# Optimization experiments

Hardware: AMD Instinct MI355X
Metric: run time of the kernel (lower is better)

The kernel has to match this reference:

```python
import jax, jax.numpy as jnp
import numpy as np

DIM = 1024
HEADS = 16
HEAD_DIM = DIM // HEADS
MAX_SEQ = 4096
BATCH = 16
POSITION = MAX_SEQ - 1


def setup_inputs() -> dict:
    key = jax.random.key(0)
    ks = jax.random.split(key, 8)
    s = 0.02  # weight init scale, typical for transformer linears
    return {
        "token": jax.random.normal(ks[0], (BATCH, 1, DIM), dtype=jnp.float32),
        "k_cache": jax.random.normal(ks[1], (BATCH, MAX_SEQ, HEADS, HEAD_DIM), dtype=jnp.float32),
        "v_cache": jax.random.normal(ks[2], (BATCH, MAX_SEQ, HEADS, HEAD_DIM), dtype=jnp.float32),
        "Wq": jax.random.normal(ks[3], (DIM, DIM), dtype=jnp.float32) * s,
        "Wk": jax.random.normal(ks[4], (DIM, DIM), dtype=jnp.float32) * s,
        "Wv": jax.random.normal(ks[5], (DIM, DIM), dtype=jnp.float32) * s,
        "Wo": jax.random.normal(ks[6], (DIM, DIM), dtype=jnp.float32) * s,
        "position": POSITION,
    }


def reference(token, k_cache, v_cache, Wq, Wk, Wv, Wo, position):
    # Decode step: single-query attention against KV cache (FlexDecodingModule.decode).
    B = token.shape[0]
    # QKV projections (torch Linear: x @ W.T), bias=False
    q = (token @ Wq.T).reshape(B, 1, HEADS, HEAD_DIM)
    k = (token @ Wk.T).reshape(B, 1, HEADS, HEAD_DIM)
    v = (token @ Wv.T).reshape(B, 1, HEADS, HEAD_DIM)
    # Inline KV-cache append at `position` (static python int)
    kc = k_cache.at[:, position].set(k[:, 0])
    vc = v_cache.at[:, position].set(v[:, 0])
    past_k = kc[:, : position + 1]  # [B, L, H, D]
    past_v = vc[:, : position + 1]
    # Causal score_mod with offset=position, q_idx=0 => all kv_idx<=position visible (no mask)
    scale = 1.0 / np.sqrt(HEAD_DIM).astype(np.float32)
    scores = jnp.einsum("bqhd,bkhd->bhqk", q, past_k) * scale  # [B, H, 1, L]
    attn = jax.nn.softmax(scores, axis=-1)
    out = jnp.einsum("bhqk,bkhd->bqhd", attn, past_v)  # [B, 1, H, D]
    out = out.reshape(B, 1, DIM)
    return out @ Wo.T
```

## Files before the change

kernel.cpp:

```cpp
#include <hip/hip_runtime.h>
#include <hip/hip_bf16.h>
#include <math.h>

#define DIM 1024
#define HEADS 16
#define HEAD_DIM 64
#define MAXSEQ 4096
#define BATCH 16
#define CHUNK 1024
#define NCHUNK (MAXSEQ / CHUNK)

__global__ __launch_bounds__(256) void qkv_proj(
    const float* __restrict__ token,
    const float* __restrict__ Wq, const float* __restrict__ Wk,
    const float* __restrict__ Wv,
    float* __restrict__ out ) {
  __shared__ float tok[BATCH * DIM];
  for (int idx = threadIdx.x; idx < BATCH * DIM; idx += 256)
    tok[idx] = token[idx];
  __syncthreads();

  const float* W = (blockIdx.y == 0) ? Wq : ((blockIdx.y == 1) ? Wk : Wv);
  float* o = out + (size_t)blockIdx.y * BATCH * DIM;

  const int wave = threadIdx.x >> 6;
  const int lane = threadIdx.x & 63;
  const int i0 = blockIdx.x * 16 + wave * 4;

  float acc[4][16];
#pragma unroll
  for (int ii = 0; ii < 4; ++ii)
#pragma unroll
    for (int b = 0; b < 16; ++b) acc[ii][b] = 0.f;

  for (int t = 0; t < 16; ++t) {
    const int j = t * 64 + lane;
    float tk[16];
#pragma unroll
    for (int b = 0; b < 16; ++b) tk[b] = tok[b * DIM + j];
#pragma unroll
    for (int ii = 0; ii < 4; ++ii) {
      const float w = W[(size_t)(i0 + ii) * DIM + j];
#pragma unroll
      for (int b = 0; b < 16; ++b) acc[ii][b] = fmaf(w, tk[b], acc[ii][b]);
    }
  }

#pragma unroll
  for (int ii = 0; ii < 4; ++ii)
#pragma unroll
    for (int b = 0; b < 16; ++b) {
      float v = acc[ii][b];
#pragma unroll
      for (int m = 32; m >= 1; m >>= 1) v += __shfl_xor(v, m);
      if (lane == 0) o[(size_t)b * DIM + i0 + ii] = v;
    }
}

__global__ __launch_bounds__(256) void attn_partial(
    const float* __restrict__ kc, const float* __restrict__ vc,
    const float* __restrict__ qkv, const int* __restrict__ pos_p,
    float* __restrict__ part) {
  const int c = blockIdx.x, h = blockIdx.y, b = blockIdx.z;
  const int tid = threadIdx.x;
  const int wave = tid >> 6, lane = tid & 63;
  const int quarter = lane >> 4, lq = lane & 15;
  const int pos = pos_p[0];
  const int nk = pos + 1;
  const int s0 = c * CHUNK;

  const float* q = qkv + (size_t)b * DIM + h * HEAD_DIM;
  const float* knew = qkv + 1 * BATCH * DIM + (size_t)b * DIM + h * HEAD_DIM;
  const float* vnew = qkv + 2 * BATCH * DIM + (size_t)b * DIM + h * HEAD_DIM;
  const float* kbase = kc + (size_t)b * MAXSEQ * DIM + h * HEAD_DIM;
  const float* vbase = vc + (size_t)b * MAXSEQ * DIM + h * HEAD_DIM;

  const float scale = 0.125f;
  float4 q4 = *(const float4*)(q + lq * 4);
  q4.x *= scale; q4.y *= scale; q4.z *= scale; q4.w *= scale;

  __shared__ float sc[CHUNK];
  __shared__ float wred[4];
  __shared__ __align__(16) float vout[4][64];

#pragma unroll 4
  for (int it = 0; it < 64; ++it) {
    const int sl = wave * 256 + it * 4 + quarter;
    const int s = s0 + sl;
    const bool valid = (s < nk);
    float d = 0.f;
    if (valid) {
      const float* krow = (s == pos) ? knew : (kbase + (size_t)s * DIM);
      const float4 k4 = *(const float4*)(krow + lq * 4);
      d = q4.x * k4.x + q4.y * k4.y + q4.z * k4.z + q4.w * k4.w;
    }
    d += __shfl_xor(d, 1);
    d += __shfl_xor(d, 2);
    d += __shfl_xor(d, 4);
    d += __shfl_xor(d, 8);
    if (lq == 0) sc[sl] = valid ? d : -INFINITY;
  }
  __syncthreads();

  float lm = -INFINITY;
#pragma unroll
  for (int r = 0; r < 4; ++r) lm = fmaxf(lm, sc[tid + r * 256]);
#pragma unroll
  for (int m = 32; m >= 1; m >>= 1) lm = fmaxf(lm, __shfl_xor(lm, m));
  if (lane == 0) wred[wave] = lm;
  __syncthreads();
  const float m = fmaxf(fmaxf(wred[0], wred[1]), fmaxf(wred[2], wred[3]));
  __syncthreads();

  float lsum = 0.f;
#pragma unroll
  for (int r = 0; r < 4; ++r) {
    const int idx = tid + r * 256;
    const float s = sc[idx];
    const float p = (s == -INFINITY) ? 0.f : __expf(s - m);
    lsum += p;
    sc[idx] = p;
  }
#pragma unroll
  for (int mm = 32; mm >= 1; mm >>= 1) lsum += __shfl_xor(lsum, mm);
  __syncthreads();
  if (lane == 0) wred[wave] = lsum;
  __syncthreads();
  const float ltot = wred[0] + wred[1] + wred[2] + wred[3];

  float4 a4 = make_float4(0.f, 0.f, 0.f, 0.f);
#pragma unroll 4
  for (int it = 0; it < 64; ++it) {
    const int sl = wave * 256 + it * 4 + quarter;
    const int s = s0 + sl;
    if (s < nk) {
      const float* vrow = (s == pos) ? vnew : (vbase + (size_t)s * DIM);
      const float4 v4 = *(const float4*)(vrow + lq * 4);
      const float p = sc[sl];
      a4.x = fmaf(p, v4.x, a4.x);
      a4.y = fmaf(p, v4.y, a4.y);
      a4.z = fmaf(p, v4.z, a4.z);
      a4.w = fmaf(p, v4.w, a4.w);
    }
  }
  a4.x += __shfl_xor(a4.x, 16); a4.x += __shfl_xor(a4.x, 32);
  a4.y += __shfl_xor(a4.y, 16); a4.y += __shfl_xor(a4.y, 32);
  a4.z += __shfl_xor(a4.z, 16); a4.z += __shfl_xor(a4.z, 32);
  a4.w += __shfl_xor(a4.w, 16); a4.w += __shfl_xor(a4.w, 32);
  if (quarter == 0) *(float4*)(&vout[wave][lq * 4]) = a4;
  __syncthreads();

  const size_t base = (((size_t)(b * HEADS + h)) * NCHUNK + c) * 66;
  if (tid < 64) {
    const float a = vout[0][tid] + vout[1][tid] + vout[2][tid] + vout[3][tid];
    part[base + 2 + tid] = a;
  }
  if (tid == 0) { part[base] = m; part[base + 1] = ltot; }
}

__global__ __launch_bounds__(64) void attn_combine(
    const float* __restrict__ part, float* __restrict__ attn) {
  const int bh = blockIdx.x;
  const int b = bh >> 4, h = bh & 15;
  const int d = threadIdx.x;
  const float* p0 = part + (size_t)bh * NCHUNK * 66;
  float M = -INFINITY;
#pragma unroll
  for (int c = 0; c < NCHUNK; ++c) M = fmaxf(M, p0[c * 66]);
  float L = 0.f, o = 0.f;
#pragma unroll
  for (int c = 0; c < NCHUNK; ++c) {
    const float mc = p0[c * 66];
    if (mc > -INFINITY) {
      const float w = __expf(mc - M);
      L += p0[c * 66 + 1] * w;
      o = fmaf(p0[c * 66 + 2 + d], w, o);
    }
  }
  attn[(size_t)b * DIM + h * HEAD_DIM + d] = o / L;
}

__global__ __launch_bounds__(256) void o_proj(
    const float* __restrict__ attn, const float* __restrict__ Wo,
    float* __restrict__ out) {
  __shared__ float tok[BATCH * DIM];
  for (int idx = threadIdx.x; idx < BATCH * DIM; idx += 256)
    tok[idx] = attn[idx];
  __syncthreads();

  const int wave = threadIdx.x >> 6;
  const int lane = threadIdx.x & 63;
  const int i0 = blockIdx.x * 16 + wave * 4;

  float acc[4][16];
#pragma unroll
  for (int ii = 0; ii < 4; ++ii)
#pragma unroll
    for (int b = 0; b < 16; ++b) acc[ii][b] = 0.f;

  for (int t = 0; t < 16; ++t) {
    const int j = t * 64 + lane;
    float tk[16];
#pragma unroll
    for (int b = 0; b < 16; ++b) tk[b] = tok[b * DIM + j];
#pragma unroll
    for (int ii = 0; ii < 4; ++ii) {
      const float w = Wo[(size_t)(i0 + ii) * DIM + j];
#pragma unroll
      for (int b = 0; b < 16; ++b) acc[ii][b] = fmaf(w, tk[b], acc[ii][b]);
    }
  }

#pragma unroll
  for (int ii = 0; ii < 4; ++ii)
#pragma unroll
    for (int b = 0; b < 16; ++b) {
      float v = acc[ii][b];
#pragma unroll
      for (int m = 32; m >= 1; m >>= 1) v += __shfl_xor(v, m);
      if (lane == 0) out[(size_t)b * DIM + i0 + ii] = v;
    }
}

extern "C" void kernel_launch(void* const* d_in, const int* in_sizes, int n_in,
                              void* d_out, int out_size, void* d_ws, size_t ws_size,
                              hipStream_t stream) {
  const float* token = (const float*)d_in[0];
  const float* kc = (const float*)d_in[1];
  const float* vc = (const float*)d_in[2];
  const float* Wq = (const float*)d_in[3];
  const float* Wk = (const float*)d_in[4];
  const float* Wv = (const float*)d_in[5];
  const float* Wv_ = (const float*)d_in[5];
  const float* Wo = (const float*)d_in[6];
  const int* pos = (const int*)d_in[7];
  float* out = (float*)d_out;
  float* ws = (float*)d_ws;

  float* qkv = ws;
  float* part = ws + 3 * BATCH * DIM;
  float* attn = part + (size_t)BATCH * HEADS * NCHUNK * 66;

  hipLaunchKernelGGL(qkv_proj, dim3(64, 3), dim3(256), 0, stream,
                     token, Wq, Wk, Wv, qkv);
  hipLaunchKernelGGL(attn_partial, dim3(NCHUNK, HEADS, BATCH), dim3(256), 0,
                     stream, kc, vc, qkv, pos, part);
  hipLaunchKernelGGL(attn_combine, dim3(BATCH * HEADS), dim3(64), 0, stream,
                     part, attn);
  hipLaunchKernelGGL(o_proj, dim3(64), dim3(256), 0, stream, attn, Wo, out);
  (void)Wv_; (void)in_sizes; (void)n_in; (void)out_size; (void)ws_size;
}
```

Before: 160.1 us.

## Restructure attention partials so each block covers all heads over short contiguous chunks

The split-KV attention kernel now gives each block one batch element and a 64-row chunk across all 16 heads, instead of one head over a 1024-row chunk. Each thread handles one float4 of a full 4KB cache row, so every row load is one contiguous 4KB read rather than a 256B slice strided by the row pitch. Softmax reductions now run per head within 16-lane groups using a padded shared score tile, which drops the cross-wave reductions and several barriers. The cost is 16 times more partial results (per chunk, per head) for the combine kernel to merge, plus a larger workspace, and fewer rows in flight per thread.

```diff
diff --git a/kernel.cpp b/kernel.cpp
--- a/kernel.cpp
+++ b/kernel.cpp
@@ -7,7 +7,7 @@
 #define HEAD_DIM 64
 #define MAXSEQ 4096
 #define BATCH 16
-#define CHUNK 1024
+#define CHUNK 64
 #define NCHUNK (MAXSEQ / CHUNK)
 
 __global__ __launch_bounds__(256) void qkv_proj(
@@ -61,101 +61,88 @@
     const float* __restrict__ kc, const float* __restrict__ vc,
     const float* __restrict__ qkv, const int* __restrict__ pos_p,
     float* __restrict__ part) {
-  const int c = blockIdx.x, h = blockIdx.y, b = blockIdx.z;
-  const int tid = threadIdx.x;
-  const int wave = tid >> 6, lane = tid & 63;
-  const int quarter = lane >> 4, lq = lane & 15;
+  const int c = blockIdx.x, b = blockIdx.y;
+  const int t = threadIdx.x;
+  const int h = t >> 4, lq = t & 15;
   const int pos = pos_p[0];
   const int nk = pos + 1;
   const int s0 = c * CHUNK;
 
-  const float* q = qkv + (size_t)b * DIM + h * HEAD_DIM;
-  const float* knew = qkv + 1 * BATCH * DIM + (size_t)b * DIM + h * HEAD_DIM;
-  const float* vnew = qkv + 2 * BATCH * DIM + (size_t)b * DIM + h * HEAD_DIM;
-  const float* kbase = kc + (size_t)b * MAXSEQ * DIM + h * HEAD_DIM;
-  const float* vbase = vc + (size_t)b * MAXSEQ * DIM + h * HEAD_DIM;
+  const float* qp   = qkv + (size_t)b * DIM;
+  const float* knew = qkv + (size_t)BATCH * DIM + (size_t)b * DIM;
+  const float* vnew = qkv + 2 * (size_t)BATCH * DIM + (size_t)b * DIM;
+  const float* kbase = kc + (size_t)b * MAXSEQ * DIM;
+  const float* vbase = vc + (size_t)b * MAXSEQ * DIM;
 
   const float scale = 0.125f;
-  float4 q4 = *(const float4*)(q + lq * 4);
+  float4 q4 = *(const float4*)(qp + 4 * t);
   q4.x *= scale; q4.y *= scale; q4.z *= scale; q4.w *= scale;
 
-  __shared__ float sc[CHUNK];
-  __shared__ float wred[4];
-  __shared__ __align__(16) float vout[4][64];
+  __shared__ float sc[CHUNK][17];
 
 #pragma unroll 4
-  for (int it = 0; it < 64; ++it) {
-    const int sl = wave * 256 + it * 4 + quarter;
-    const int s = s0 + sl;
+  for (int i = 0; i < CHUNK; ++i) {
+    const int s = s0 + i;
     const bool valid = (s < nk);
     float d = 0.f;
     if (valid) {
       const float* krow = (s == pos) ? knew : (kbase + (size_t)s * DIM);
-      const float4 k4 = *(const float4*)(krow + lq * 4);
+      const float4 k4 = *(const float4*)(krow + 4 * t);
       d = q4.x * k4.x + q4.y * k4.y + q4.z * k4.z + q4.w * k4.w;
-    }
-    d += __shfl_xor(d, 1);
-    d += __shfl_xor(d, 2);
-    d += __shfl_xor(d, 4);
-    d += __shfl_xor(d, 8);
-    if (lq == 0) sc[sl] = valid ? d : -INFINITY;
-  }
-  __syncthreads();
-
-  float lm = -INFINITY;
-#pragma unroll
-  for (int r = 0; r < 4; ++r) lm = fmaxf(lm, sc[tid + r * 256]);
-#pragma unroll
-  for (int m = 32; m >= 1; m >>= 1) lm = fmaxf(lm, __shfl_xor(lm, m));
-  if (lane == 0) wred[wave] = lm;
-  __syncthreads();
-  const float m = fmaxf(fmaxf(wred[0], wred[1]), fmaxf(wred[2], wred[3]));
-  __syncthreads();
-
-  float lsum = 0.f;
-#pragma unroll
-  for (int r = 0; r < 4; ++r) {
-    const int idx = tid + r * 256;
-    const float s = sc[idx];
-    const float p = (s == -INFINITY) ? 0.f : __expf(s - m);
-    lsum += p;
-    sc[idx] = p;
-  }
-#pragma unroll
-  for (int mm = 32; mm >= 1; mm >>= 1) lsum += __shfl_xor(lsum, mm);
-  __syncthreads();
-  if (lane == 0) wred[wave] = lsum;
-  __syncthreads();
-  const float ltot = wred[0] + wred[1] + wred[2] + wred[3];
+      d += __shfl_xor(d, 1);
+      d += __shfl_xor(d, 2);
+      d += __shfl_xor(d, 4);
+      d += __shfl_xor(d, 8);
+    }
+    if (lq == 0) sc[i][h] = valid ? d : -INFINITY;
+  }
+  __syncthreads();
+
+  float m = -INFINITY;
+#pragma unroll
+  for (int r = 0; r < CHUNK / 16; ++r)
+    m = fmaxf(m, sc[lq * (CHUNK / 16) + r][h]);
+  m = fmaxf(m, __shfl_xor(m, 1));
+  m = fmaxf(m, __shfl_xor(m, 2));
+  m = fmaxf(m, __shfl_xor(m, 4));
+  m = fmaxf(m, __shfl_xor(m, 8));
+
+  float l = 0.f;
+#pragma unroll
+  for (int r = 0; r < CHUNK / 16; ++r) {
+    const int i = lq * (CHUNK / 16) + r;
+    const float sv = sc[i][h];
+    const float p = (sv == -INFINITY) ? 0.f : __expf(sv - m);
+    l += p;
+    sc[i][h] = p;
+  }
+  l += __shfl_xor(l, 1);
+  l += __shfl_xor(l, 2);
+  l += __shfl_xor(l, 4);
+  l += __shfl_xor(l, 8);
+  __syncthreads();
 
   float4 a4 = make_float4(0.f, 0.f, 0.f, 0.f);
 #pragma unroll 4
-  for (int it = 0; it < 64; ++it) {
-    const int sl = wave * 256 + it * 4 + quarter;
-    const int s = s0 + sl;
+  for (int i = 0; i < CHUNK; ++i) {
+    const int s = s0 + i;
     if (s < nk) {
       const float* vrow = (s == pos) ? vnew : (vbase + (size_t)s * DIM);
-      const float4 v4 = *(const float4*)(vrow + lq * 4);
-      const float p = sc[sl];
+      const float4 v4 = *(const float4*)(vrow + 4 * t);
+      const float p = sc[i][h];
       a4.x = fmaf(p, v4.x, a4.x);
       a4.y = fmaf(p, v4.y, a4.y);
       a4.z = fmaf(p, v4.z, a4.z);
       a4.w = fmaf(p, v4.w, a4.w);
     }
   }
-  a4.x += __shfl_xor(a4.x, 16); a4.x += __shfl_xor(a4.x, 32);
-  a4.y += __shfl_xor(a4.y, 16); a4.y += __shfl_xor(a4.y, 32);
-  a4.z += __shfl_xor(a4.z, 16); a4.z += __shfl_xor(a4.z, 32);
-  a4.w += __shfl_xor(a4.w, 16); a4.w += __shfl_xor(a4.w, 32);
-  if (quarter == 0) *(float4*)(&vout[wave][lq * 4]) = a4;
-  __syncthreads();
 
   const size_t base = (((size_t)(b * HEADS + h)) * NCHUNK + c) * 66;
-  if (tid < 64) {
-    const float a = vout[0][tid] + vout[1][tid] + vout[2][tid] + vout[3][tid];
-    part[base + 2 + tid] = a;
-  }
-  if (tid == 0) { part[base] = m; part[base + 1] = ltot; }
+  part[base + 2 + lq * 4 + 0] = a4.x;
+  part[base + 2 + lq * 4 + 1] = a4.y;
+  part[base + 2 + lq * 4 + 2] = a4.z;
+  part[base + 2 + lq * 4 + 3] = a4.w;
+  if (lq == 0) { part[base] = m; part[base + 1] = l; }
 }
 
 __global__ __launch_bounds__(64) void attn_combine(
@@ -168,7 +155,7 @@
 #pragma unroll
   for (int c = 0; c < NCHUNK; ++c) M = fmaxf(M, p0[c * 66]);
   float L = 0.f, o = 0.f;
-#pragma unroll
+#pragma unroll 8
   for (int c = 0; c < NCHUNK; ++c) {
     const float mc = p0[c * 66];
     if (mc > -INFINITY) {
@@ -231,7 +218,6 @@
   const float* Wq = (const float*)d_in[3];
   const float* Wk = (const float*)d_in[4];
   const float* Wv = (const float*)d_in[5];
-  const float* Wv_ = (const float*)d_in[5];
   const float* Wo = (const float*)d_in[6];
   const int* pos = (const int*)d_in[7];
   float* out = (float*)d_out;
@@ -243,10 +229,10 @@
 
   hipLaunchKernelGGL(qkv_proj, dim3(64, 3), dim3(256), 0, stream,
                      token, Wq, Wk, Wv, qkv);
-  hipLaunchKernelGGL(attn_partial, dim3(NCHUNK, HEADS, BATCH), dim3(256), 0,
+  hipLaunchKernelGGL(attn_partial, dim3(NCHUNK, BATCH), dim3(256), 0,
                      stream, kc, vc, qkv, pos, part);
   hipLaunchKernelGGL(attn_combine, dim3(BATCH * HEADS), dim3(64), 0, stream,
                      part, attn);
   hipLaunchKernelGGL(o_proj, dim3(64), dim3(256), 0, stream, attn, Wo, out);
-  (void)Wv_; (void)in_sizes; (void)n_in; (void)out_size; (void)ws_size;
-}
+  (void)in_sizes; (void)n_in; (void)out_size; (void)ws_size;
+}
```

New measurement: 176.2 us. 10.0% more time.
